# Optimization experiments

Hardware: AMD Instinct MI355X
Metric: run time of the kernel (lower is better)

Reference implementation:

```python
import jax, jax.numpy as jnp
import numpy as np

V, E, L, T, H, B = 8124, 1024, 24, 512, 16, 2
S = E // H
DFF = E * 8 // 3  # 2730
EPS = 1e-5
SCALE = 1.0 / np.sqrt(E)  # note: 1/sqrt(emb_dim), as in the source


def _pe():
    # sinusoidal positional encoding [T, E]
    pos = jnp.arange(T, dtype=jnp.float32)[:, None]
    div = jnp.exp(jnp.arange(0, E, 2, dtype=jnp.float32) * (-np.log(10000.0) / E))
    pe = jnp.zeros((T, E), jnp.float32)
    pe = pe.at[:, 0::2].set(jnp.sin(pos * div))
    pe = pe.at[:, 1::2].set(jnp.cos(pos * div))
    return pe


def _rms(x, g):
    # NOTE: source takes the mean over the WHOLE tensor (no dim arg)
    rms = jnp.sqrt(jnp.mean(x.astype(jnp.float32) ** 2) + EPS)
    return (x / rms * g).astype(x.dtype)


def setup_inputs() -> dict:
    key = jax.random.key(0)
    ks = jax.random.split(key, 9)
    def w(k, shape):
        return jax.random.normal(k, shape, jnp.float32) * 0.02
    return {
        "tokens": jax.random.randint(ks[0], (B, T), 0, V),
        "emb_table": w(ks[1], (V, E)),
        "Wqkv": w(ks[2], (L, E, 3 * E)), "bqkv": jnp.zeros((L, 3 * E), jnp.float32),
        "Wo": w(ks[3], (L, E, E)), "bo": jnp.zeros((L, E), jnp.float32),
        "W1": w(ks[4], (L, E, DFF)), "b1": jnp.zeros((L, DFF), jnp.float32),
        "W3": w(ks[5], (L, E, DFF)), "b3": jnp.zeros((L, DFF), jnp.float32),
        "W2": w(ks[6], (L, DFF, E)), "b2": jnp.zeros((L, E), jnp.float32),
        "g_mha": jnp.ones((L, E), jnp.float32),
        "g_ff": jnp.ones((L, E), jnp.float32),
        "g_final": jnp.ones((E,), jnp.float32),
        "Wout": w(ks[7], (E, V)), "bout": jnp.zeros((V,), jnp.float32),
    }


def reference(tokens, emb_table, Wqkv, bqkv, Wo, bo, W1, b1, W3, b3, W2, b2,
              g_mha, g_ff, g_final, Wout, bout):
    x = emb_table[tokens] + _pe()[None]  # [B,T,E]
    mask = jnp.tril(jnp.ones((T, T), bool))

    def block(x, p):
        wqkv, bq, wo, bo_, w1, b1_, w3, b3_, w2, b2_, gm, gf = p
        # --- causal MHA ---
        y = _rms(x, gm)
        qkv = (y @ wqkv + bq).reshape(B, T, H, 3, S)
        q = qkv[..., 0, :].transpose(0, 2, 1, 3)  # [B,H,T,S]
        k = qkv[..., 1, :].transpose(0, 2, 1, 3)
        v = qkv[..., 2, :].transpose(0, 2, 1, 3)
        attn = jnp.einsum('bhqd,bhkd->bhqk', q, k).astype(jnp.float32) * SCALE
        attn = jnp.where(mask, attn, -jnp.inf)
        attn = jax.nn.softmax(attn, axis=-1).astype(x.dtype)
        y = jnp.einsum('bhqk,bhkd->bhqd', attn, v)
        y = y.transpose(0, 2, 1, 3).reshape(B, T, E)
        x = x + (y @ wo + bo_)
        # --- SwiGLU FFN ---
        h = _rms(x, gf)
        u = h @ w1 + b1_
        u = u * jax.nn.sigmoid(u) * (h @ w3 + b3_)
        return x + (u @ w2 + b2_), None

    x, _ = jax.lax.scan(block, x, (Wqkv, bqkv, Wo, bo, W1, b1, W3, b3, W2, b2, g_mha, g_ff))
    return _rms(x, g_final) @ Wout + bout  # [B,T,V]
```

## Files before the change

kernel.cpp:

```cpp
#include <hip/hip_runtime.h>
#include <hip/hip_bf16.h>
#include <math.h>

#define EDIM   1024
#define TSEQ   512
#define NBATCH 2
#define NHEAD  16
#define HDIM   64
#define NLAYER 24
#define VOCAB  8124
#define DFFDIM 2730
#define DPAD   2752
#define MTOK   (NBATCH*TSEQ)
#define NELEM  (MTOK*EDIM)
#define EPSF   1e-5f
#define SCALEF (1.0f/32.0f)
#define NEGBIG (-1e30f)

typedef __bf16 bf16x8 __attribute__((ext_vector_type(8)));
typedef __bf16 bf16x4 __attribute__((ext_vector_type(4)));
typedef float  f32x4  __attribute__((ext_vector_type(4)));

#define MFMA(a, b, c) __builtin_amdgcn_mfma_f32_16x16x32_bf16((a), (b), (c), 0, 0, 0)

__device__ __forceinline__ void gl_lds16(const __bf16* g, __bf16* l) {
  __builtin_amdgcn_global_load_lds(
      (const __attribute__((address_space(1))) void*)g,
      (__attribute__((address_space(3))) void*)l, 16, 0, 0);
}
template <int N> __device__ __forceinline__ void vmwait() {
  asm volatile("s_waitcnt vmcnt(%0)" :: "n"(N) : "memory");
}
__device__ __forceinline__ void lgkm_barrier() {
  asm volatile("s_waitcnt lgkmcnt(0)" ::: "memory");
  __builtin_amdgcn_s_barrier();
}

__global__ __launch_bounds__(256) void k_embed(const int* __restrict__ tok,
                                               const float* __restrict__ emb,
                                               float* __restrict__ x) {
  const int bt = blockIdx.x;
  const int t  = bt & (TSEQ - 1);
  const int tk = tok[bt];
  const float* er = emb + (size_t)tk * EDIM;
  float* xr = x + (size_t)bt * EDIM;
  for (int e = threadIdx.x * 4; e < EDIM; e += 256 * 4) {
    float4 v = *(const float4*)(er + e);
    float vv[4] = {v.x, v.y, v.z, v.w};
    float ou[4];
#pragma unroll
    for (int j = 0; j < 4; ++j) {
      int ee = e + j;
      int i2 = ee & ~1;
      float freq = expf(-(float)i2 * (9.210340371976184f / 1024.0f));
      float ang  = (float)t * freq;
      ou[j] = vv[j] + ((ee & 1) ? cosf(ang) : sinf(ang));
    }
    *(float4*)(xr + e) = make_float4(ou[0], ou[1], ou[2], ou[3]);
  }
}

__global__ __launch_bounds__(256) void k_red1f(float* __restrict__ x,
                                               const float* __restrict__ pb,
                                               const float* __restrict__ bias,
                                               float* __restrict__ part) {
  float s = 0.f;
  const bool fold = (pb != nullptr);
  for (int i = (blockIdx.x * 256 + threadIdx.x) * 4; i < NELEM; i += 256 * 256 * 4) {
    float4 v = *(const float4*)(x + i);
    if (fold) {
#pragma unroll
      for (int z = 0; z < 4; ++z) {
        float4 a = *(const float4*)(pb + (size_t)z * NELEM + i);
        v.x += a.x; v.y += a.y; v.z += a.z; v.w += a.w;
      }
      float4 c = *(const float4*)(bias + (i & (EDIM - 1)));
      v.x += c.x; v.y += c.y; v.z += c.z; v.w += c.w;
      *(float4*)(x + i) = v;
    }
    s += v.x * v.x + v.y * v.y + v.z * v.z + v.w * v.w;
  }
#pragma unroll
  for (int o = 32; o > 0; o >>= 1) s += __shfl_down(s, o);
  __shared__ float sm[4];
  if ((threadIdx.x & 63) == 0) sm[threadIdx.x >> 6] = s;
  __syncthreads();
  if (threadIdx.x == 0) part[blockIdx.x] = sm[0] + sm[1] + sm[2] + sm[3];
}

__global__ __launch_bounds__(256) void k_rms2(const float* __restrict__ x,
                                              const float* __restrict__ g,
                                              const float* __restrict__ part,
                                              __bf16* __restrict__ y) {
  float s = part[threadIdx.x];
#pragma unroll
  for (int o = 32; o > 0; o >>= 1) s += __shfl_down(s, o);
  __shared__ float sm[4];
  if ((threadIdx.x & 63) == 0) sm[threadIdx.x >> 6] = s;
  __syncthreads();
  const float sc = 1.0f / sqrtf((sm[0] + sm[1] + sm[2] + sm[3]) / (float)NELEM + EPSF);
  const int i = (blockIdx.x * 256 + threadIdx.x) * 4;
  float4 v  = *(const float4*)(x + i);
  float4 gv = *(const float4*)(g + (i & (EDIM - 1)));
  bf16x4 o4 = {(__bf16)(v.x * sc * gv.x), (__bf16)(v.y * sc * gv.y),
               (__bf16)(v.z * sc * gv.z), (__bf16)(v.w * sc * gv.w)};
  *(bf16x4*)(y + i) = o4;
}

__device__ __forceinline__ void conv_tile(const float* __restrict__ src,
                                          __bf16* __restrict__ dst,
                                          int K, int N, int Kpad, int tk, int tn) {
  __shared__ float st[64][65];
  const int k0 = tk << 6, n0 = tn << 6;
  const int tid = threadIdx.x;
  const int r0 = tid >> 4, c4 = (tid & 15) << 2;
#pragma unroll
  for (int i = 0; i < 4; ++i) {
    const int r = r0 + i * 16;
    const int k = k0 + r;
    float4 v = make_float4(0.f, 0.f, 0.f, 0.f);
    if (k < K) {
      const float* sp = src + (size_t)k * N + n0 + c4;
      if (n0 + c4 + 3 < N) v = *(const float4*)sp;
      else {
        if (n0 + c4 + 0 < N) v.x = sp[0];
        if (n0 + c4 + 1 < N) v.y = sp[1];
        if (n0 + c4 + 2 < N) v.z = sp[2];
        if (n0 + c4 + 3 < N) v.w = sp[3];
      }
    }
    st[r][c4 + 0] = v.x; st[r][c4 + 1] = v.y; st[r][c4 + 2] = v.z; st[r][c4 + 3] = v.w;
  }
  __syncthreads();
#pragma unroll
  for (int i = 0; i < 4; ++i) {
    const int rr = r0 + i * 16;
    bf16x4 o = {(__bf16)st[c4 + 0][rr], (__bf16)st[c4 + 1][rr],
                (__bf16)st[c4 + 2][rr], (__bf16)st[c4 + 3][rr]};
    *(bf16x4*)&dst[(size_t)(n0 + rr) * Kpad + k0 + c4] = o;
  }
}

__global__ __launch_bounds__(256) void k_convAll(const float* __restrict__ Wqkv,
                                                 const float* __restrict__ Wo,
                                                 const float* __restrict__ W1,
                                                 const float* __restrict__ W3,
                                                 const float* __restrict__ W2w,
                                                 __bf16* qkvT, __bf16* woT,
                                                 __bf16* w1T, __bf16* w3T, __bf16* w2T) {
  int b = blockIdx.x;
  const int l = b / 3088; b -= l * 3088;
  if (b < 768) {
    conv_tile(Wqkv + (size_t)l * 1024 * 3072, qkvT + (size_t)l * 3072 * 1024,
              1024, 3072, 1024, b / 48, b % 48);
  } else if (b < 1024) {
    int t = b - 768;
    conv_tile(Wo + (size_t)l * 1024 * 1024, woT + (size_t)l * 1024 * 1024,
              1024, 1024, 1024, t / 16, t % 16);
  } else if (b < 1712) {
    int t = b - 1024;
    conv_tile(W1 + (size_t)l * 1024 * DFFDIM, w1T + (size_t)l * DPAD * 1024,
              1024, DFFDIM, 1024, t / 43, t % 43);
  } else if (b < 2400) {
    int t = b - 1712;
    conv_tile(W3 + (size_t)l * 1024 * DFFDIM, w3T + (size_t)l * DPAD * 1024,
              1024, DFFDIM, 1024, t / 43, t % 43);
  } else {
    int t = b - 2400;
    conv_tile(W2w + (size_t)l * DFFDIM * 1024, w2T + (size_t)l * 1024 * DPAD,
              DFFDIM, 1024, DPAD, t / 16, t % 16);
  }
}

__global__ __launch_bounds__(256) void k_convH(const float* __restrict__ Wout,
                                               __bf16* __restrict__ WoutT) {
  conv_tile(Wout, WoutT, 1024, VOCAB, 1024, blockIdx.x >> 7, blockIdx.x & 127);
}

template <int BN, int MODE>
__global__ __launch_bounds__(256) void mm(
    const __bf16* __restrict__ A, const __bf16* __restrict__ B0w,
    const __bf16* __restrict__ B1w,
    const float* __restrict__ bias0, const float* __restrict__ bias1,
    float* __restrict__ po, __bf16* __restrict__ ob,
    __bf16* __restrict__ qout, __bf16* __restrict__ kout, __bf16* __restrict__ vout,
    int N, int lda, int ldb, int Ktot) {
  constexpr int DUAL = (MODE == 2) ? 2 : 1;
  constexpr int FN = BN / 32;
  constexpr int WNC = BN / 2;
  __shared__ __bf16 As[2][8][128][8];
  __shared__ __bf16 Bs[2][DUAL][8][BN][8];
  const int tid = threadIdx.x, lane = tid & 63, wave = tid >> 6;
  const int m0 = blockIdx.y << 7, n0 = blockIdx.x * BN;
  const int wm0 = (wave >> 1) * 64, wn0 = (wave & 1) * WNC;
  const int lr = lane & 15, kh = lane >> 4;

  const int ktiles = Ktot >> 6;
  const int nt0 = (ktiles + gridDim.z - 1) / gridDim.z;
  const int tbeg = blockIdx.z * nt0;
  const int tend = (ktiles < tbeg + nt0) ? ktiles : (tbeg + nt0);
  const int nt = tend - tbeg;

  f32x4 acc[DUAL][4][FN];
#pragma unroll
  for (int d = 0; d < DUAL; ++d)
#pragma unroll
    for (int mi = 0; mi < 4; ++mi)
#pragma unroll
      for (int fn = 0; fn < FN; ++fn) acc[d][mi][fn] = (f32x4){0.f, 0.f, 0.f, 0.f};

  auto STAGE = [&](int buf, int t) {
    const int k0 = (tbeg + t) << 6;
#pragma unroll
    for (int i = 0; i < 4; ++i) {
      const int d = i * 256 + tid;
      gl_lds16(A + (size_t)(m0 + (d & 127)) * lda + k0 + (d >> 7) * 8,
               &As[buf][d >> 7][d & 127][0]);
    }
    if (BN == 128) {
#pragma unroll
      for (int i = 0; i < 4; ++i) {
        const int d = i * 256 + tid;
        gl_lds16(B0w + (size_t)(n0 + (d & 127)) * ldb + k0 + (d >> 7) * 8,
                 &Bs[buf][0][d >> 7][d & 127][0]);
      }
    } else {
#pragma unroll
      for (int i = 0; i < 2; ++i) {
        const int d = i * 256 + tid;
        gl_lds16(B0w + (size_t)(n0 + (d & 63)) * ldb + k0 + (d >> 6) * 8,
                 &Bs[buf][0][d >> 6][d & 63][0]);
      }
      if (DUAL == 2) {
#pragma unroll
        for (int i = 0; i < 2; ++i) {
          const int d = i * 256 + tid;
          gl_lds16(B1w + (size_t)(n0 + (d & 63)) * ldb + k0 + (d >> 6) * 8,
                   &Bs[buf][DUAL - 1][d >> 6][d & 63][0]);
        }
      }
    }
  };
  auto COMP = [&](int buf) {
#pragma unroll
    for (int ks = 0; ks < 2; ++ks) {
      const int kidx = ks * 4 + kh;
      bf16x8 af[4];
#pragma unroll
      for (int mi = 0; mi < 4; ++mi)
        af[mi] = *(const bf16x8*)&As[buf][kidx][wm0 + mi * 16 + lr][0];
#pragma unroll
      for (int d = 0; d < DUAL; ++d)
#pragma unroll
        for (int fn = 0; fn < FN; ++fn) {
          bf16x8 bfr = *(const bf16x8*)&Bs[buf][d][kidx][wn0 + fn * 16 + lr][0];
#pragma unroll
          for (int mi = 0; mi < 4; ++mi)
            acc[d][mi][fn] = MFMA(af[mi], bfr, acc[d][mi][fn]);
        }
    }
  };

  STAGE(0, 0);
  int cur = 0;
  for (int t = 0; t < nt - 1; ++t) {
    STAGE(cur ^ 1, t + 1);
    vmwait<8>();
    __builtin_amdgcn_s_barrier();
    COMP(cur);
    __builtin_amdgcn_s_barrier();
    cur ^= 1;
  }
  vmwait<0>();
  __builtin_amdgcn_s_barrier();
  COMP(cur);

#pragma unroll
  for (int mi = 0; mi < 4; ++mi)
#pragma unroll
    for (int fn = 0; fn < FN; ++fn) {
      const int col = n0 + wn0 + fn * 16 + lr;
      if (MODE == 0) {
        const float bs = bias0[col];
        const int h = col / (3 * HDIM);
        const int rsel = (col >> 6) % 3;
        const int s2 = col & (HDIM - 1);
#pragma unroll
        for (int j = 0; j < 4; ++j) {
          const int row = m0 + wm0 + mi * 16 + (kh << 2) + j;
          const int b = row >> 9, t = row & (TSEQ - 1);
          const float v = acc[0][mi][fn][j] + bs;
          if (rsel == 0)      qout[((size_t)(b * NHEAD + h) * TSEQ + t) * HDIM + s2] = (__bf16)v;
          else if (rsel == 1) kout[((size_t)(b * NHEAD + h) * TSEQ + t) * HDIM + s2] = (__bf16)v;
          else                vout[((size_t)(b * NHEAD + h) * HDIM + s2) * TSEQ + t] = (__bf16)v;
        }
      } else if (MODE == 1) {
        float* pz = po + (size_t)blockIdx.z * NELEM;
#pragma unroll
        for (int j = 0; j < 4; ++j) {
          const int row = m0 + wm0 + mi * 16 + (kh << 2) + j;
          pz[(size_t)row * EDIM + col] = acc[0][mi][fn][j];
        }
      } else if (MODE == 2) {
        const bool ok = col < N;
        const float bb1 = ok ? bias0[col] : 0.f;
        const float bb3 = ok ? bias1[col] : 0.f;
#pragma unroll
        for (int j = 0; j < 4; ++j) {
          const int row = m0 + wm0 + mi * 16 + (kh << 2) + j;
          float v = 0.f;
          if (ok) {
            const float a1v = acc[0][mi][fn][j] + bb1;
            const float a3v = acc[DUAL - 1][mi][fn][j] + bb3;
            v = a1v * (1.0f / (1.0f + __expf(-a1v))) * a3v;
          }
          ob[(size_t)row * DPAD + col] = (__bf16)v;
        }
      } else {
        if (col < N) {
          const float bs = bias0[col];
#pragma unroll
          for (int j = 0; j < 4; ++j) {
            const int row = m0 + wm0 + mi * 16 + (kh << 2) + j;
            po[(size_t)row * N + col] = acc[0][mi][fn][j] + bs;
          }
        }
      }
    }
}

__global__ __launch_bounds__(256) void k_flash(const __bf16* __restrict__ qbuf,
                                               const __bf16* __restrict__ kbuf,
                                               const __bf16* __restrict__ vbufT,
                                               __bf16* __restrict__ y2) {
  const int qt = blockIdx.x, bh = blockIdx.y;
  const int b = bh >> 4, h = bh & 15;
  const int m0 = qt << 6;
  const __bf16* qp = qbuf  + (size_t)bh * TSEQ * HDIM;
  const __bf16* kp = kbuf  + (size_t)bh * TSEQ * HDIM;
  const __bf16* vp = vbufT + (size_t)bh * HDIM * TSEQ;
  __shared__ __bf16 Qs[8][64][8], Ks[2][8][64][8], Vs[2][8][64][8], Ps[8][64][8];
  __shared__ float wmax[2][64], wsum[2][64];
  const int tid = threadIdx.x, lane = tid & 63, wave = tid >> 6;
  const int wm = (wave >> 1) << 5, wn = (wave & 1) << 5;
  const int lr = lane & 15, kh = lane >> 4;

  auto STAGE_KV = [&](int kt2, int buf) {
    const int n0s = kt2 << 6;
#pragma unroll
    for (int i = 0; i < 2; ++i) {
      const int d = i * 256 + tid;
      const int kb2 = d >> 6, row = d & 63;
      gl_lds16(kp + (size_t)(n0s + row) * HDIM + kb2 * 8, &Ks[buf][kb2][row][0]);
      gl_lds16(vp + (size_t)row * TSEQ + n0s + kb2 * 8, &Vs[buf][kb2][row][0]);
    }
  };

#pragma unroll
  for (int i = 0; i < 2; ++i) {
    const int d = i * 256 + tid;
    const int kb2 = d >> 6, row = d & 63;
    gl_lds16(qp + (size_t)(m0 + row) * HDIM + kb2 * 8, &Qs[kb2][row][0]);
  }
  STAGE_KV(0, 0);

  float m_[2][4], l_[2][4];
#pragma unroll
  for (int mi = 0; mi < 2; ++mi)
#pragma unroll
    for (int j = 0; j < 4; ++j) { m_[mi][j] = NEGBIG; l_[mi][j] = 0.f; }
  f32x4 o00 = {0,0,0,0}, o01 = {0,0,0,0}, o10 = {0,0,0,0}, o11 = {0,0,0,0};

  int cur = 0;
  for (int kt = 0; kt <= qt; ++kt) {
    const int n0 = kt << 6;
    if (kt < qt) {
      STAGE_KV(kt + 1, cur ^ 1);
      vmwait<4>();
    } else {
      vmwait<0>();
    }
    __builtin_amdgcn_s_barrier();

    f32x4 s00 = {0,0,0,0}, s01 = {0,0,0,0}, s10 = {0,0,0,0}, s11 = {0,0,0,0};
#pragma unroll
    for (int ks = 0; ks < 2; ++ks) {
      const int kidx = ks * 4 + kh;
      bf16x8 a0 = *(const bf16x8*)&Qs[kidx][wm + lr][0];
      bf16x8 a1 = *(const bf16x8*)&Qs[kidx][wm + 16 + lr][0];
      bf16x8 b0 = *(const bf16x8*)&Ks[cur][kidx][wn + lr][0];
      bf16x8 b1 = *(const bf16x8*)&Ks[cur][kidx][wn + 16 + lr][0];
      s00 = MFMA(a0, b0, s00); s01 = MFMA(a0, b1, s01);
      s10 = MFMA(a1, b0, s10); s11 = MFMA(a1, b1, s11);
    }
    float pv_[2][2][4];
#pragma unroll
    for (int mi = 0; mi < 2; ++mi)
#pragma unroll
      for (int j = 0; j < 4; ++j) {
        const int grow = m0 + wm + mi * 16 + (kh << 2) + j;
        float best = NEGBIG;
#pragma unroll
        for (int ni = 0; ni < 2; ++ni) {
          f32x4 sfr = (mi == 0) ? (ni == 0 ? s00 : s01) : (ni == 0 ? s10 : s11);
          const int gcol = n0 + wn + ni * 16 + lr;
          float t = sfr[j] * SCALEF;
          if (gcol > grow) t = NEGBIG;
          pv_[mi][ni][j] = t;
          best = fmaxf(best, t);
        }
        float v = best;
        v = fmaxf(v, __shfl_xor(v, 1)); v = fmaxf(v, __shfl_xor(v, 2));
        v = fmaxf(v, __shfl_xor(v, 4)); v = fmaxf(v, __shfl_xor(v, 8));
        wmax[wave & 1][wm + mi * 16 + (kh << 2) + j] = v;
      }
    lgkm_barrier();

    float alpha[2][4];
#pragma unroll
    for (int mi = 0; mi < 2; ++mi)
#pragma unroll
      for (int j = 0; j < 4; ++j) {
        const int rl = wm + mi * 16 + (kh << 2) + j;
        const float tmax = fmaxf(wmax[0][rl], wmax[1][rl]);
        const float mn = fmaxf(m_[mi][j], tmax);
        alpha[mi][j] = __expf(m_[mi][j] - mn);
        m_[mi][j] = mn;
        float rs = 0.f;
#pragma unroll
        for (int ni = 0; ni < 2; ++ni) {
          const float p = __expf(pv_[mi][ni][j] - mn);
          pv_[mi][ni][j] = p;
          rs += p;
        }
        rs += __shfl_xor(rs, 1); rs += __shfl_xor(rs, 2);
        rs += __shfl_xor(rs, 4); rs += __shfl_xor(rs, 8);
        wsum[wave & 1][rl] = rs;
      }
#pragma unroll
    for (int mi = 0; mi < 2; ++mi)
#pragma unroll
      for (int ni = 0; ni < 2; ++ni)
#pragma unroll
        for (int j = 0; j < 4; ++j) {
          const int prow = wm + mi * 16 + (kh << 2) + j;
          const int pcol = wn + ni * 16 + lr;
          Ps[pcol >> 3][prow][pcol & 7] = (__bf16)pv_[mi][ni][j];
        }
    lgkm_barrier();

#pragma unroll
    for (int mi = 0; mi < 2; ++mi)
#pragma unroll
      for (int j = 0; j < 4; ++j) {
        const int rl = wm + mi * 16 + (kh << 2) + j;
        l_[mi][j] = l_[mi][j] * alpha[mi][j] + wsum[0][rl] + wsum[1][rl];
      }
#pragma unroll
    for (int j = 0; j < 4; ++j) {
      o00[j] *= alpha[0][j]; o01[j] *= alpha[0][j];
      o10[j] *= alpha[1][j]; o11[j] *= alpha[1][j];
    }
#pragma unroll
    for (int ks = 0; ks < 2; ++ks) {
      const int kidx = ks * 4 + kh;
      bf16x8 a0 = *(const bf16x8*)&Ps[kidx][wm + lr][0];
      bf16x8 a1 = *(const bf16x8*)&Ps[kidx][wm + 16 + lr][0];
      bf16x8 b0 = *(const bf16x8*)&Vs[cur][kidx][wn + lr][0];
      bf16x8 b1 = *(const bf16x8*)&Vs[cur][kidx][wn + 16 + lr][0];
      o00 = MFMA(a0, b0, o00); o01 = MFMA(a0, b1, o01);
      o10 = MFMA(a1, b0, o10); o11 = MFMA(a1, b1, o11);
    }
    __builtin_amdgcn_s_barrier();
    cur ^= 1;
  }

#pragma unroll
  for (int mi = 0; mi < 2; ++mi)
#pragma unroll
    for (int ni = 0; ni < 2; ++ni) {
      f32x4 oo = (mi == 0) ? (ni == 0 ? o00 : o01) : (ni == 0 ? o10 : o11);
      const int col = wn + ni * 16 + lr;
#pragma unroll
      for (int j = 0; j < 4; ++j) {
        const int row = m0 + wm + mi * 16 + (kh << 2) + j;
        y2[((size_t)(b * TSEQ) + row) * EDIM + h * HDIM + col] = (__bf16)(oo[j] / l_[mi][j]);
      }
    }
}

extern "C" void kernel_launch(void* const* d_in, const int* in_sizes, int n_in,
                              void* d_out, int out_size, void* d_ws, size_t ws_size,
                              hipStream_t stream) {
  const int*   tokens  = (const int*)d_in[0];
  const float* emb     = (const float*)d_in[1];
  const float* Wqkv    = (const float*)d_in[2];
  const float* bqkv    = (const float*)d_in[3];
  const float* Wo      = (const float*)d_in[4];
  const float* bo      = (const float*)d_in[5];
  const float* W1      = (const float*)d_in[6];
  const float* b1      = (const float*)d_in[7];
  const float* W3      = (const float*)d_in[8];
  const float* b3      = (const float*)d_in[9];
  const float* W2w     = (const float*)d_in[10];
  const float* b2      = (const float*)d_in[11];
  const float* g_mha   = (const float*)d_in[12];
  const float* g_ff    = (const float*)d_in[13];
  const float* g_final = (const float*)d_in[14];
  const float* Wout    = (const float*)d_in[15];
  const float* bout    = (const float*)d_in[16];
  float* out = (float*)d_out;

  char* base = (char*)d_ws;
  size_t off = 0;
  auto alloc = [&](size_t bytes) { char* p = base + off; off = (off + bytes + 255) & ~(size_t)255; return p; };
  float*  x    = (float*)alloc(4u << 20);
  float*  part = (float*)alloc(2048);
  __bf16* ybf  = (__bf16*)alloc(2u << 20);
  __bf16* qbf  = (__bf16*)alloc(2u << 20);
  __bf16* kbf  = (__bf16*)alloc(2u << 20);
  __bf16* vbT  = (__bf16*)alloc(2u << 20);
  __bf16* y2bf = (__bf16*)alloc(2u << 20);
  __bf16* ubf  = (__bf16*)alloc((size_t)MTOK * DPAD * 2);
  float*  pbuf = (float*)alloc((size_t)4 * NELEM * 4);
  __bf16* WoutT = (__bf16*)alloc((size_t)8192 * 1024 * 2);
  __bf16* qkvT = (__bf16*)alloc((size_t)NLAYER * 3072 * 1024 * 2);
  __bf16* woT  = (__bf16*)alloc((size_t)NLAYER * 1024 * 1024 * 2);
  __bf16* w1T  = (__bf16*)alloc((size_t)NLAYER * DPAD * 1024 * 2);
  __bf16* w3T  = (__bf16*)alloc((size_t)NLAYER * DPAD * 1024 * 2);
  __bf16* w2T  = (__bf16*)alloc((size_t)NLAYER * 1024 * DPAD * 2);

  k_embed<<<MTOK, 256, 0, stream>>>(tokens, emb, x);
  k_convAll<<<NLAYER * 3088, 256, 0, stream>>>(Wqkv, Wo, W1, W3, W2w,
                                               qkvT, woT, w1T, w3T, w2T);
  k_convH<<<2048, 256, 0, stream>>>(Wout, WoutT);

  const float* pend_bias = nullptr;
  for (int l = 0; l < NLAYER; ++l) {
    k_red1f<<<256, 256, 0, stream>>>(x, pend_bias ? pbuf : nullptr, pend_bias, part);
    k_rms2<<<1024, 256, 0, stream>>>(x, g_mha + (size_t)l * EDIM, part, ybf);
    mm<128, 0><<<dim3(24, 8, 1), 256, 0, stream>>>(
        ybf, qkvT + (size_t)l * 3072 * 1024, nullptr,
        bqkv + (size_t)l * 3 * EDIM, nullptr,
        nullptr, nullptr, qbf, kbf, vbT, 3072, 1024, 1024, 1024);
    k_flash<<<dim3(8, 32), 256, 0, stream>>>(qbf, kbf, vbT, y2bf);
    mm<128, 1><<<dim3(8, 8, 4), 256, 0, stream>>>(
        y2bf, woT + (size_t)l * 1024 * 1024, nullptr, nullptr, nullptr,
        pbuf, nullptr, nullptr, nullptr, nullptr, 1024, 1024, 1024, 1024);
    k_red1f<<<256, 256, 0, stream>>>(x, pbuf, bo + (size_t)l * EDIM, part);
    k_rms2<<<1024, 256, 0, stream>>>(x, g_ff + (size_t)l * EDIM, part, ybf);
    mm<64, 2><<<dim3(43, 8, 1), 256, 0, stream>>>(
        ybf, w1T + (size_t)l * DPAD * 1024, w3T + (size_t)l * DPAD * 1024,
        b1 + (size_t)l * DFFDIM, b3 + (size_t)l * DFFDIM,
        nullptr, ubf, nullptr, nullptr, nullptr, DFFDIM, 1024, 1024, 1024);
    mm<128, 1><<<dim3(8, 8, 4), 256, 0, stream>>>(
        ubf, w2T + (size_t)l * 1024 * DPAD, nullptr, nullptr, nullptr,
        pbuf, nullptr, nullptr, nullptr, nullptr, 1024, DPAD, DPAD, DPAD);
    pend_bias = b2 + (size_t)l * EDIM;
  }

  k_red1f<<<256, 256, 0, stream>>>(x, pbuf, pend_bias, part);
  k_rms2<<<1024, 256, 0, stream>>>(x, g_final, part, ybf);
  mm<128, 3><<<dim3(64, 8, 1), 256, 0, stream>>>(
      ybf, WoutT, nullptr, bout, nullptr,
      out, nullptr, nullptr, nullptr, nullptr, VOCAB, 1024, 1024, 1024);
}
```

Before: 4.124 ms.

## Fold RMSNorm gains into weights and fuse normalization into GEMM A-loads

The per-element RMSNorm gain is folded into the bf16 weight transpose, and the global scalar RMS scale is applied in the GEMM epilogue. The GEMMs now read the fp32 residual directly, converting to bf16 while staging into a swizzled LDS layout. This removes the separate k_rms2 kernel and its bf16 intermediate in every layer. Split-K is reduced from 4 to 2 with BN=64 tiles, and the weight conversion writes 8-wide bf16 stores; the fused A path uses register staging with full waits, which may reduce load/compute overlap.

New measurement: 4.220 ms. +2.3%, slower.

```diff
diff --git a/kernel.cpp b/kernel.cpp
--- a/kernel.cpp
+++ b/kernel.cpp
@@ -62,6 +62,7 @@
 
 __global__ __launch_bounds__(256) void k_red1f(float* __restrict__ x,
                                                const float* __restrict__ pb,
+                                               int np,
                                                const float* __restrict__ bias,
                                                float* __restrict__ part) {
   float s = 0.f;
@@ -69,8 +70,7 @@
   for (int i = (blockIdx.x * 256 + threadIdx.x) * 4; i < NELEM; i += 256 * 256 * 4) {
     float4 v = *(const float4*)(x + i);
     if (fold) {
-#pragma unroll
-      for (int z = 0; z < 4; ++z) {
+      for (int z = 0; z < np; ++z) {
         float4 a = *(const float4*)(pb + (size_t)z * NELEM + i);
         v.x += a.x; v.y += a.y; v.z += a.z; v.w += a.w;
       }
@@ -88,56 +88,49 @@
   if (threadIdx.x == 0) part[blockIdx.x] = sm[0] + sm[1] + sm[2] + sm[3];
 }
 
-__global__ __launch_bounds__(256) void k_rms2(const float* __restrict__ x,
-                                              const float* __restrict__ g,
-                                              const float* __restrict__ part,
-                                              __bf16* __restrict__ y) {
-  float s = part[threadIdx.x];
-#pragma unroll
-  for (int o = 32; o > 0; o >>= 1) s += __shfl_down(s, o);
-  __shared__ float sm[4];
-  if ((threadIdx.x & 63) == 0) sm[threadIdx.x >> 6] = s;
-  __syncthreads();
-  const float sc = 1.0f / sqrtf((sm[0] + sm[1] + sm[2] + sm[3]) / (float)NELEM + EPSF);
-  const int i = (blockIdx.x * 256 + threadIdx.x) * 4;
-  float4 v  = *(const float4*)(x + i);
-  float4 gv = *(const float4*)(g + (i & (EDIM - 1)));
-  bf16x4 o4 = {(__bf16)(v.x * sc * gv.x), (__bf16)(v.y * sc * gv.y),
-               (__bf16)(v.z * sc * gv.z), (__bf16)(v.w * sc * gv.w)};
-  *(bf16x4*)(y + i) = o4;
-}
-
 __device__ __forceinline__ void conv_tile(const float* __restrict__ src,
+                                          const float* __restrict__ gk,
                                           __bf16* __restrict__ dst,
                                           int K, int N, int Kpad, int tk, int tn) {
   __shared__ float st[64][65];
   const int k0 = tk << 6, n0 = tn << 6;
   const int tid = threadIdx.x;
-  const int r0 = tid >> 4, c4 = (tid & 15) << 2;
-#pragma unroll
-  for (int i = 0; i < 4; ++i) {
-    const int r = r0 + i * 16;
-    const int k = k0 + r;
-    float4 v = make_float4(0.f, 0.f, 0.f, 0.f);
-    if (k < K) {
-      const float* sp = src + (size_t)k * N + n0 + c4;
-      if (n0 + c4 + 3 < N) v = *(const float4*)sp;
-      else {
-        if (n0 + c4 + 0 < N) v.x = sp[0];
-        if (n0 + c4 + 1 < N) v.y = sp[1];
-        if (n0 + c4 + 2 < N) v.z = sp[2];
-        if (n0 + c4 + 3 < N) v.w = sp[3];
-      }
-    }
-    st[r][c4 + 0] = v.x; st[r][c4 + 1] = v.y; st[r][c4 + 2] = v.z; st[r][c4 + 3] = v.w;
+  {
+    const int r0 = tid >> 4, c4 = (tid & 15) << 2;
+#pragma unroll
+    for (int i = 0; i < 4; ++i) {
+      const int r = r0 + i * 16;
+      const int k = k0 + r;
+      float4 v = make_float4(0.f, 0.f, 0.f, 0.f);
+      if (k < K) {
+        const float* sp = src + (size_t)k * N + n0 + c4;
+        if (n0 + c4 + 3 < N) v = *(const float4*)sp;
+        else {
+          if (n0 + c4 + 0 < N) v.x = sp[0];
+          if (n0 + c4 + 1 < N) v.y = sp[1];
+          if (n0 + c4 + 2 < N) v.z = sp[2];
+          if (n0 + c4 + 3 < N) v.w = sp[3];
+        }
+        if (gk) {
+          const float gv = gk[k];
+          v.x *= gv; v.y *= gv; v.z *= gv; v.w *= gv;
+        }
+      }
+      st[r][c4 + 0] = v.x; st[r][c4 + 1] = v.y; st[r][c4 + 2] = v.z; st[r][c4 + 3] = v.w;
+    }
   }
   __syncthreads();
-#pragma unroll
-  for (int i = 0; i < 4; ++i) {
-    const int rr = r0 + i * 16;
-    bf16x4 o = {(__bf16)st[c4 + 0][rr], (__bf16)st[c4 + 1][rr],
-                (__bf16)st[c4 + 2][rr], (__bf16)st[c4 + 3][rr]};
-    *(bf16x4*)&dst[(size_t)(n0 + rr) * Kpad + k0 + c4] = o;
+  {
+    const int nl0 = tid >> 3, c8 = (tid & 7) << 3;
+#pragma unroll
+    for (int i = 0; i < 2; ++i) {
+      const int nl = nl0 + i * 32;
+      bf16x8 o = {(__bf16)st[c8 + 0][nl], (__bf16)st[c8 + 1][nl],
+                  (__bf16)st[c8 + 2][nl], (__bf16)st[c8 + 3][nl],
+                  (__bf16)st[c8 + 4][nl], (__bf16)st[c8 + 5][nl],
+                  (__bf16)st[c8 + 6][nl], (__bf16)st[c8 + 7][nl]};
+      *(bf16x8*)&dst[(size_t)(n0 + nl) * Kpad + k0 + c8] = o;
+    }
   }
 }
 
@@ -146,53 +139,57 @@
                                                  const float* __restrict__ W1,
                                                  const float* __restrict__ W3,
                                                  const float* __restrict__ W2w,
+                                                 const float* __restrict__ g_mha,
+                                                 const float* __restrict__ g_ff,
                                                  __bf16* qkvT, __bf16* woT,
                                                  __bf16* w1T, __bf16* w3T, __bf16* w2T) {
   int b = blockIdx.x;
   const int l = b / 3088; b -= l * 3088;
   if (b < 768) {
-    conv_tile(Wqkv + (size_t)l * 1024 * 3072, qkvT + (size_t)l * 3072 * 1024,
-              1024, 3072, 1024, b / 48, b % 48);
+    conv_tile(Wqkv + (size_t)l * 1024 * 3072, g_mha + (size_t)l * EDIM,
+              qkvT + (size_t)l * 3072 * 1024, 1024, 3072, 1024, b / 48, b % 48);
   } else if (b < 1024) {
     int t = b - 768;
-    conv_tile(Wo + (size_t)l * 1024 * 1024, woT + (size_t)l * 1024 * 1024,
-              1024, 1024, 1024, t / 16, t % 16);
+    conv_tile(Wo + (size_t)l * 1024 * 1024, nullptr,
+              woT + (size_t)l * 1024 * 1024, 1024, 1024, 1024, t / 16, t % 16);
   } else if (b < 1712) {
     int t = b - 1024;
-    conv_tile(W1 + (size_t)l * 1024 * DFFDIM, w1T + (size_t)l * DPAD * 1024,
-              1024, DFFDIM, 1024, t / 43, t % 43);
+    conv_tile(W1 + (size_t)l * 1024 * DFFDIM, g_ff + (size_t)l * EDIM,
+              w1T + (size_t)l * DPAD * 1024, 1024, DFFDIM, 1024, t / 43, t % 43);
   } else if (b < 2400) {
     int t = b - 1712;
-    conv_tile(W3 + (size_t)l * 1024 * DFFDIM, w3T + (size_t)l * DPAD * 1024,
-              1024, DFFDIM, 1024, t / 43, t % 43);
+    conv_tile(W3 + (size_t)l * 1024 * DFFDIM, g_ff + (size_t)l * EDIM,
+              w3T + (size_t)l * DPAD * 1024, 1024, DFFDIM, 1024, t / 43, t % 43);
   } else {
     int t = b - 2400;
-    conv_tile(W2w + (size_t)l * DFFDIM * 1024, w2T + (size_t)l * 1024 * DPAD,
-              DFFDIM, 1024, DPAD, t / 16, t % 16);
+    conv_tile(W2w + (size_t)l * DFFDIM * 1024, nullptr,
+              w2T + (size_t)l * 1024 * DPAD, DFFDIM, 1024, DPAD, t / 16, t % 16);
   }
 }
 
 __global__ __launch_bounds__(256) void k_convH(const float* __restrict__ Wout,
+                                               const float* __restrict__ g_final,
                                                __bf16* __restrict__ WoutT) {
-  conv_tile(Wout, WoutT, 1024, VOCAB, 1024, blockIdx.x >> 7, blockIdx.x & 127);
-}
-
-template <int BN, int MODE>
+  conv_tile(Wout, g_final, WoutT, 1024, VOCAB, 1024, blockIdx.x >> 7, blockIdx.x & 127);
+}
+
+template <int BN, int MODE, int FUSE>
 __global__ __launch_bounds__(256) void mm(
-    const __bf16* __restrict__ A, const __bf16* __restrict__ B0w,
-    const __bf16* __restrict__ B1w,
+    const __bf16* __restrict__ A, const float* __restrict__ Af,
+    const __bf16* __restrict__ B0w, const __bf16* __restrict__ B1w,
     const float* __restrict__ bias0, const float* __restrict__ bias1,
+    const float* __restrict__ part,
     float* __restrict__ po, __bf16* __restrict__ ob,
     __bf16* __restrict__ qout, __bf16* __restrict__ kout, __bf16* __restrict__ vout,
     int N, int lda, int ldb, int Ktot) {
   constexpr int DUAL = (MODE == 2) ? 2 : 1;
   constexpr int FN = BN / 32;
-  constexpr int WNC = BN / 2;
+  constexpr int BL = (BN == 128) ? 4 : 2 * DUAL;
   __shared__ __bf16 As[2][8][128][8];
   __shared__ __bf16 Bs[2][DUAL][8][BN][8];
   const int tid = threadIdx.x, lane = tid & 63, wave = tid >> 6;
   const int m0 = blockIdx.y << 7, n0 = blockIdx.x * BN;
-  const int wm0 = (wave >> 1) * 64, wn0 = (wave & 1) * WNC;
+  const int wm0 = (wave >> 1) * 64, wn0 = (wave & 1) * (BN / 2);
   const int lr = lane & 15, kh = lane >> 4;
 
   const int ktiles = Ktot >> 6;
@@ -209,7 +206,29 @@
 #pragma unroll
       for (int fn = 0; fn < FN; ++fn) acc[d][mi][fn] = (f32x4){0.f, 0.f, 0.f, 0.f};
 
-  auto STAGE = [&](int buf, int t) {
+  float4 ar[4][2];
+  auto LOADA = [&](int t) {
+    const int k0 = (tbeg + t) << 6;
+#pragma unroll
+    for (int i = 0; i < 4; ++i) {
+      const int d = i * 256 + tid;
+      const int row = d >> 3, kb = d & 7;
+      const float* ap = Af + (size_t)(m0 + row) * lda + k0 + kb * 8;
+      ar[i][0] = *(const float4*)ap; ar[i][1] = *(const float4*)(ap + 4);
+    }
+  };
+  auto DSWA = [&](int buf) {
+#pragma unroll
+    for (int i = 0; i < 4; ++i) {
+      const int d = i * 256 + tid;
+      const int row = d >> 3, kb = d & 7;
+      float4 a = ar[i][0], b = ar[i][1];
+      bf16x8 w = {(__bf16)a.x, (__bf16)a.y, (__bf16)a.z, (__bf16)a.w,
+                  (__bf16)b.x, (__bf16)b.y, (__bf16)b.z, (__bf16)b.w};
+      *(bf16x8*)&As[buf][kb][row ^ kb][0] = w;
+    }
+  };
+  auto STAGEA_G = [&](int buf, int t) {
     const int k0 = (tbeg + t) << 6;
 #pragma unroll
     for (int i = 0; i < 4; ++i) {
@@ -217,6 +236,9 @@
       gl_lds16(A + (size_t)(m0 + (d & 127)) * lda + k0 + (d >> 7) * 8,
                &As[buf][d >> 7][d & 127][0]);
     }
+  };
+  auto STAGEB = [&](int buf, int t) {
+    const int k0 = (tbeg + t) << 6;
     if (BN == 128) {
 #pragma unroll
       for (int i = 0; i < 4; ++i) {
@@ -247,8 +269,10 @@
       const int kidx = ks * 4 + kh;
       bf16x8 af[4];
 #pragma unroll
-      for (int mi = 0; mi < 4; ++mi)
-        af[mi] = *(const bf16x8*)&As[buf][kidx][wm0 + mi * 16 + lr][0];
+      for (int mi = 0; mi < 4; ++mi) {
+        const int r = wm0 + mi * 16 + lr;
+        af[mi] = *(const bf16x8*)&As[buf][kidx][FUSE ? (r ^ kidx) : r][0];
+      }
 #pragma unroll
       for (int d = 0; d < DUAL; ++d)
 #pragma unroll
@@ -261,19 +285,45 @@
     }
   };
 
-  STAGE(0, 0);
   int cur = 0;
-  for (int t = 0; t < nt - 1; ++t) {
-    STAGE(cur ^ 1, t + 1);
-    vmwait<8>();
-    __builtin_amdgcn_s_barrier();
+  if (FUSE) {
+    LOADA(0); STAGEB(0, 0); DSWA(0);
+    asm volatile("s_waitcnt lgkmcnt(0)" ::: "memory");
+    vmwait<0>(); __builtin_amdgcn_s_barrier();
+    for (int t = 0; t < nt - 1; ++t) {
+      LOADA(t + 1);
+      STAGEB(cur ^ 1, t + 1);
+      COMP(cur);
+      DSWA(cur ^ 1);
+      asm volatile("s_waitcnt lgkmcnt(0)" ::: "memory");
+      vmwait<0>(); __builtin_amdgcn_s_barrier();
+      cur ^= 1;
+    }
     COMP(cur);
-    __builtin_amdgcn_s_barrier();
-    cur ^= 1;
-  }
-  vmwait<0>();
-  __builtin_amdgcn_s_barrier();
-  COMP(cur);
+  } else {
+    STAGEA_G(0, 0); STAGEB(0, 0);
+    for (int t = 0; t < nt - 1; ++t) {
+      STAGEA_G(cur ^ 1, t + 1); STAGEB(cur ^ 1, t + 1);
+      vmwait<4 + BL>();
+      __builtin_amdgcn_s_barrier();
+      COMP(cur);
+      __builtin_amdgcn_s_barrier();
+      cur ^= 1;
+    }
+    vmwait<0>(); __builtin_amdgcn_s_barrier();
+    COMP(cur);
+  }
+
+  float sc = 1.0f;
+  if (FUSE) {
+    __shared__ float smr[4];
+    float s = part[tid];
+#pragma unroll
+    for (int o = 32; o > 0; o >>= 1) s += __shfl_down(s, o);
+    if ((tid & 63) == 0) smr[tid >> 6] = s;
+    __syncthreads();
+    sc = 1.0f / sqrtf((smr[0] + smr[1] + smr[2] + smr[3]) / (float)NELEM + EPSF);
+  }
 
 #pragma unroll
   for (int mi = 0; mi < 4; ++mi)
@@ -289,7 +339,7 @@
         for (int j = 0; j < 4; ++j) {
           const int row = m0 + wm0 + mi * 16 + (kh << 2) + j;
           const int b = row >> 9, t = row & (TSEQ - 1);
-          const float v = acc[0][mi][fn][j] + bs;
+          const float v = acc[0][mi][fn][j] * sc + bs;
           if (rsel == 0)      qout[((size_t)(b * NHEAD + h) * TSEQ + t) * HDIM + s2] = (__bf16)v;
           else if (rsel == 1) kout[((size_t)(b * NHEAD + h) * TSEQ + t) * HDIM + s2] = (__bf16)v;
           else                vout[((size_t)(b * NHEAD + h) * HDIM + s2) * TSEQ + t] = (__bf16)v;
@@ -310,8 +360,8 @@
           const int row = m0 + wm0 + mi * 16 + (kh << 2) + j;
           float v = 0.f;
           if (ok) {
-            const float a1v = acc[0][mi][fn][j] + bb1;
-            const float a3v = acc[DUAL - 1][mi][fn][j] + bb3;
+            const float a1v = acc[0][mi][fn][j] * sc + bb1;
+            const float a3v = acc[DUAL - 1][mi][fn][j] * sc + bb3;
             v = a1v * (1.0f / (1.0f + __expf(-a1v))) * a3v;
           }
           ob[(size_t)row * DPAD + col] = (__bf16)v;
@@ -322,7 +372,7 @@
 #pragma unroll
           for (int j = 0; j < 4; ++j) {
             const int row = m0 + wm0 + mi * 16 + (kh << 2) + j;
-            po[(size_t)row * N + col] = acc[0][mi][fn][j] + bs;
+            po[(size_t)row * N + col] = acc[0][mi][fn][j] * sc + bs;
           }
         }
       }
@@ -516,13 +566,12 @@
   auto alloc = [&](size_t bytes) { char* p = base + off; off = (off + bytes + 255) & ~(size_t)255; return p; };
   float*  x    = (float*)alloc(4u << 20);
   float*  part = (float*)alloc(2048);
-  __bf16* ybf  = (__bf16*)alloc(2u << 20);
   __bf16* qbf  = (__bf16*)alloc(2u << 20);
   __bf16* kbf  = (__bf16*)alloc(2u << 20);
   __bf16* vbT  = (__bf16*)alloc(2u << 20);
   __bf16* y2bf = (__bf16*)alloc(2u << 20);
   __bf16* ubf  = (__bf16*)alloc((size_t)MTOK * DPAD * 2);
-  float*  pbuf = (float*)alloc((size_t)4 * NELEM * 4);
+  float*  pbuf = (float*)alloc((size_t)2 * NELEM * 4);
   __bf16* WoutT = (__bf16*)alloc((size_t)8192 * 1024 * 2);
   __bf16* qkvT = (__bf16*)alloc((size_t)NLAYER * 3072 * 1024 * 2);
   __bf16* woT  = (__bf16*)alloc((size_t)NLAYER * 1024 * 1024 * 2);
@@ -532,36 +581,36 @@
 
   k_embed<<<MTOK, 256, 0, stream>>>(tokens, emb, x);
   k_convAll<<<NLAYER * 3088, 256, 0, stream>>>(Wqkv, Wo, W1, W3, W2w,
+                                               g_mha, g_ff,
                                                qkvT, woT, w1T, w3T, w2T);
-  k_convH<<<2048, 256, 0, stream>>>(Wout, WoutT);
+  k_convH<<<2048, 256, 0, stream>>>(Wout, g_final, WoutT);
 
   const float* pend_bias = nullptr;
   for (int l = 0; l < NLAYER; ++l) {
-    k_red1f<<<256, 256, 0, stream>>>(x, pend_bias ? pbuf : nullptr, pend_bias, part);
-    k_rms2<<<1024, 256, 0, stream>>>(x, g_mha + (size_t)l * EDIM, part, ybf);
-    mm<128, 0><<<dim3(24, 8, 1), 256, 0, stream>>>(
-        ybf, qkvT + (size_t)l * 3072 * 1024, nullptr,
-        bqkv + (size_t)l * 3 * EDIM, nullptr,
-        nullptr, nullptr, qbf, kbf, vbT, 3072, 1024, 1024, 1024);
+    k_red1f<<<256, 256, 0, stream>>>(x, pend_bias ? pbuf : nullptr, 2, pend_bias, part);
+    mm<64, 0, 1><<<dim3(48, 8, 1), 256, 0, stream>>>(
+        nullptr, x, qkvT + (size_t)l * 3072 * 1024, nullptr,
+        bqkv + (size_t)l * 3 * EDIM, nullptr, part,
+        nullptr, nullptr, qbf, kbf, vbT, 3072, EDIM, 1024, 1024);
     k_flash<<<dim3(8, 32), 256, 0, stream>>>(qbf, kbf, vbT, y2bf);
-    mm<128, 1><<<dim3(8, 8, 4), 256, 0, stream>>>(
-        y2bf, woT + (size_t)l * 1024 * 1024, nullptr, nullptr, nullptr,
+    mm<64, 1, 0><<<dim3(16, 8, 2), 256, 0, stream>>>(
+        y2bf, nullptr, woT + (size_t)l * 1024 * 1024, nullptr,
+        nullptr, nullptr, nullptr,
         pbuf, nullptr, nullptr, nullptr, nullptr, 1024, 1024, 1024, 1024);
-    k_red1f<<<256, 256, 0, stream>>>(x, pbuf, bo + (size_t)l * EDIM, part);
-    k_rms2<<<1024, 256, 0, stream>>>(x, g_ff + (size_t)l * EDIM, part, ybf);
-    mm<64, 2><<<dim3(43, 8, 1), 256, 0, stream>>>(
-        ybf, w1T + (size_t)l * DPAD * 1024, w3T + (size_t)l * DPAD * 1024,
-        b1 + (size_t)l * DFFDIM, b3 + (size_t)l * DFFDIM,
-        nullptr, ubf, nullptr, nullptr, nullptr, DFFDIM, 1024, 1024, 1024);
-    mm<128, 1><<<dim3(8, 8, 4), 256, 0, stream>>>(
-        ubf, w2T + (size_t)l * 1024 * DPAD, nullptr, nullptr, nullptr,
+    k_red1f<<<256, 256, 0, stream>>>(x, pbuf, 2, bo + (size_t)l * EDIM, part);
+    mm<64, 2, 1><<<dim3(43, 8, 1), 256, 0, stream>>>(
+        nullptr, x, w1T + (size_t)l * DPAD * 1024, w3T + (size_t)l * DPAD * 1024,
+        b1 + (size_t)l * DFFDIM, b3 + (size_t)l * DFFDIM, part,
+        nullptr, ubf, nullptr, nullptr, nullptr, DFFDIM, EDIM, 1024, 1024);
+    mm<64, 1, 0><<<dim3(16, 8, 2), 256, 0, stream>>>(
+        ubf, nullptr, w2T + (size_t)l * 1024 * DPAD, nullptr,
+        nullptr, nullptr, nullptr,
         pbuf, nullptr, nullptr, nullptr, nullptr, 1024, DPAD, DPAD, DPAD);
     pend_bias = b2 + (size_t)l * EDIM;
   }
 
-  k_red1f<<<256, 256, 0, stream>>>(x, pbuf, pend_bias, part);
-  k_rms2<<<1024, 256, 0, stream>>>(x, g_final, part, ybf);
-  mm<128, 3><<<dim3(64, 8, 1), 256, 0, stream>>>(
-      ybf, WoutT, nullptr, bout, nullptr,
-      out, nullptr, nullptr, nullptr, nullptr, VOCAB, 1024, 1024, 1024);
-}
+  k_red1f<<<256, 256, 0, stream>>>(x, pbuf, 2, pend_bias, part);
+  mm<128, 3, 1><<<dim3(64, 8, 1), 256, 0, stream>>>(
+      nullptr, x, WoutT, nullptr, bout, nullptr, part,
+      out, nullptr, nullptr, nullptr, nullptr, VOCAB, EDIM, 1024, 1024);
+}
```
